# Optimization experiments

Hardware: AMD Instinct MI355X
Metric: run time of the kernel (lower is better)

Reference implementation:

```python
import jax, jax.numpy as jnp
import numpy as np

B, N, C = 2, 2048, 1024
H = 16
D = C // H
HID = 4 * C
EPS = 1e-5


def layernorm(x, g, b):
    mu = jnp.mean(x, axis=-1, keepdims=True)
    var = jnp.var(x, axis=-1, keepdims=True)
    return (x - mu) * jax.lax.rsqrt(var + EPS) * g + b


def setup_inputs() -> dict:
    key = jax.random.key(0)
    ks = jax.random.split(key, 8)
    s = lambda fan_in: 1.0 / np.sqrt(fan_in)
    return {
        "x": jax.random.normal(ks[0], (B, N, C), dtype=jnp.float32),
        "ln1_g": jnp.ones((C,), jnp.float32),
        "ln1_b": jnp.zeros((C,), jnp.float32),
        "w_qkv": jax.random.normal(ks[1], (C, 3 * C), jnp.float32) * s(C),
        "w_proj": jax.random.normal(ks[2], (C, C), jnp.float32) * s(C),
        "b_proj": jnp.zeros((C,), jnp.float32),
        "ln2_g": jnp.ones((C,), jnp.float32),
        "ln2_b": jnp.zeros((C,), jnp.float32),
        "w_fc1": jax.random.normal(ks[3], (C, HID), jnp.float32) * s(C),
        "b_fc1": jnp.zeros((HID,), jnp.float32),
        "w_fc2": jax.random.normal(ks[4], (HID, C), jnp.float32) * s(HID),
        "b_fc2": jnp.zeros((C,), jnp.float32),
        "metadata": 0,
        "thw_shape": 2048,
    }


def reference(x, ln1_g, ln1_b, w_qkv, w_proj, b_proj, ln2_g, ln2_b,
              w_fc1, b_fc1, w_fc2, b_fc2, metadata, thw_shape):
    scale = 1.0 / np.sqrt(D)
    # --- attention branch (pre-norm) ---
    xn = layernorm(x, ln1_g, ln1_b)
    qkv = (xn @ w_qkv).reshape(B, N, 3, H, D)
    q = jnp.transpose(qkv[:, :, 0], (0, 2, 1, 3))  # [B,H,N,D]
    k = jnp.transpose(qkv[:, :, 1], (0, 2, 1, 3))
    v = jnp.transpose(qkv[:, :, 2], (0, 2, 1, 3))
    attn = jax.nn.softmax(jnp.einsum('bhnd,bhmd->bhnm', q, k) * scale, axis=-1)
    o = jnp.einsum('bhnm,bhmd->bhnd', attn, v)
    o = jnp.transpose(o, (0, 2, 1, 3)).reshape(B, N, C)
    x = x + (o @ w_proj + b_proj)
    # --- MLP branch (pre-norm) ---
    xn2 = layernorm(x, ln2_g, ln2_b)
    h = jax.nn.gelu(xn2 @ w_fc1 + b_fc1, approximate=False)  # torch GELU = exact erf
    x = x + (h @ w_fc2 + b_fc2)
    return x
```

## Files before the change

kernel.cpp:

```cpp
#include <hip/hip_runtime.h>

#define B_   2
#define N_   2048
#define C_   1024
#define H_   16
#define D_   64
#define HID_ 4096
#define M_   (B_ * N_)

typedef __attribute__((ext_vector_type(8))) short bf16x8;
typedef __attribute__((ext_vector_type(4))) short short4v;
typedef __attribute__((ext_vector_type(4))) float f32x4;

__device__ __forceinline__ unsigned short f2bf(float f) {
  unsigned int u = __builtin_bit_cast(unsigned int, f);
  u += 0x7fffu + ((u >> 16) & 1u);
  return (unsigned short)(u >> 16);
}
__device__ __forceinline__ float bf2f(unsigned short s) {
  unsigned int u = ((unsigned int)s) << 16;
  return __builtin_bit_cast(float, u);
}
__device__ __forceinline__ unsigned int pkbf(float lo, float hi) {
  return __builtin_amdgcn_perm(__builtin_bit_cast(unsigned int, hi),
                               __builtin_bit_cast(unsigned int, lo),
                               0x07060302u);
}

__device__ __forceinline__ void gl2lds16(const void* g, void* l) {
  __builtin_amdgcn_global_load_lds(
      (const __attribute__((address_space(1))) unsigned int*)g,
      (__attribute__((address_space(3))) unsigned int*)l, 16, 0, 0);
}

__global__ __launch_bounds__(256) void ln_kernel(const float* __restrict__ x,
                                                 const float* __restrict__ g,
                                                 const float* __restrict__ bta,
                                                 unsigned short* __restrict__ out) {
  int row  = blockIdx.x * 4 + (threadIdx.x >> 6);
  int lane = threadIdx.x & 63;
  const float* xr = x + (size_t)row * C_;
  float4 v[4];
  float s1 = 0.f, s2 = 0.f;
#pragma unroll
  for (int j = 0; j < 4; j++) {
    v[j] = *(const float4*)(xr + j * 256 + lane * 4);
    s1 += v[j].x + v[j].y + v[j].z + v[j].w;
    s2 += v[j].x * v[j].x + v[j].y * v[j].y + v[j].z * v[j].z + v[j].w * v[j].w;
  }
#pragma unroll
  for (int m = 1; m < 64; m <<= 1) { s1 += __shfl_xor(s1, m); s2 += __shfl_xor(s2, m); }
  float mu  = s1 * (1.0f / C_);
  float var = s2 * (1.0f / C_) - mu * mu;
  float rs  = rsqrtf(var + 1e-5f);
#pragma unroll
  for (int j = 0; j < 4; j++) {
    const float4 gv = *(const float4*)(g + j * 256 + lane * 4);
    const float4 bv = *(const float4*)(bta + j * 256 + lane * 4);
    ushort4 o;
    o.x = f2bf((v[j].x - mu) * rs * gv.x + bv.x);
    o.y = f2bf((v[j].y - mu) * rs * gv.y + bv.y);
    o.z = f2bf((v[j].z - mu) * rs * gv.z + bv.z);
    o.w = f2bf((v[j].w - mu) * rs * gv.w + bv.w);
    *(ushort4*)(out + (size_t)row * C_ + j * 256 + lane * 4) = o;
  }
}

__global__ __launch_bounds__(256) void wtrans_kernel(const float* __restrict__ W,
                                                     unsigned short* __restrict__ Wt,
                                                     int K, int N) {
  __shared__ float t[32][33];
  int n0 = blockIdx.x * 32, k0 = blockIdx.y * 32;
  int tx = threadIdx.x, ty = threadIdx.y;
#pragma unroll
  for (int j = 0; j < 4; j++)
    t[ty + j * 8][tx] = W[(size_t)(k0 + ty + j * 8) * N + n0 + tx];
  __syncthreads();
#pragma unroll
  for (int j = 0; j < 4; j++)
    Wt[(size_t)(n0 + ty + j * 8) * K + k0 + tx] = f2bf(t[tx][ty + j * 8]);
}

__global__ __launch_bounds__(256) void vtrans_kernel(const unsigned short* __restrict__ v,
                                                     unsigned short* __restrict__ vt) {
  __shared__ unsigned short t[32][33];
  int bh = blockIdx.z;
  int n0 = blockIdx.x * 32, d0 = blockIdx.y * 32;
  const unsigned short* src = v + (size_t)bh * N_ * D_;
  unsigned short* dst = vt + (size_t)bh * D_ * N_;
  int tx = threadIdx.x, ty = threadIdx.y;
#pragma unroll
  for (int j = 0; j < 4; j++)
    t[ty + j * 8][tx] = src[(size_t)(n0 + ty + j * 8) * D_ + d0 + tx];
  __syncthreads();
#pragma unroll
  for (int j = 0; j < 4; j++)
    dst[(size_t)(d0 + ty + j * 8) * N_ + n0 + tx] = t[tx][ty + j * 8];
}

template <int MODE, int BN>
__global__ __launch_bounds__(256) void gemm_kernel(
    const unsigned short* __restrict__ A,
    const unsigned short* __restrict__ Wt,
    const float* __restrict__ bias,
    const float* __restrict__ resid,
    float* __restrict__ outf,
    float* __restrict__ partf,
    unsigned short* __restrict__ outb0,
    unsigned short* __restrict__ outb1,
    unsigned short* __restrict__ outb2,
    int M, int N, int K) {
  constexpr int MT = (BN == 128) ? 4 : 2;
  __shared__ __align__(16) short As[128][64];
  __shared__ __align__(16) short Bs[BN][64];
  int tid = threadIdx.x;
  int w = tid >> 6, lane = tid & 63, r = lane & 15, quad = lane >> 4;
  int rowbase = (BN == 128) ? (w >> 1) * 64 : w * 32;
  int colbase = (BN == 128) ? (w & 1) * 64 : 0;
  int bM = blockIdx.y * 128, bN = blockIdx.x * BN;

  int kz   = (MODE == 3) ? blockIdx.z : 0;
  int kbeg = (MODE == 3) ? kz * (K >> 1) : 0;
  int kend = (MODE == 3) ? kbeg + (K >> 1) : K;

  int srow   = (w << 3) + (lane >> 3);
  int schunk = (lane & 7) ^ ((lane >> 3) & 7);
  const unsigned short* aP = A  + (size_t)(bM + srow) * K + schunk * 8;
  const unsigned short* bP = Wt + (size_t)(bN + srow) * K + schunk * 8;

  int pc0 = (quad ^ (r & 7)) * 8;

  f32x4 acc[MT][4];
#pragma unroll
  for (int i = 0; i < MT; i++)
#pragma unroll
    for (int j = 0; j < 4; j++) acc[i][j] = f32x4{0.f, 0.f, 0.f, 0.f};

  for (int k0 = kbeg; k0 < kend; k0 += 64) {
    __syncthreads();
#pragma unroll
    for (int p = 0; p < 4; p++)
      gl2lds16(aP + (size_t)(p * 32) * K + k0, &As[p * 32 + (w << 3)][0]);
#pragma unroll
    for (int p = 0; p < BN / 32; p++)
      gl2lds16(bP + (size_t)(p * 32) * K + k0, &Bs[p * 32 + (w << 3)][0]);
    __syncthreads();
#pragma unroll
    for (int kh = 0; kh < 2; kh++) {
      int pc = pc0 ^ (kh * 32);
      bf16x8 af[MT], bfr[4];
#pragma unroll
      for (int mt = 0; mt < MT; mt++)
        af[mt] = *(const bf16x8*)&As[rowbase + mt * 16 + r][pc];
#pragma unroll
      for (int nt = 0; nt < 4; nt++)
        bfr[nt] = *(const bf16x8*)&Bs[colbase + nt * 16 + r][pc];
#pragma unroll
      for (int mt = 0; mt < MT; mt++)
#pragma unroll
        for (int nt = 0; nt < 4; nt++)
          acc[mt][nt] = __builtin_amdgcn_mfma_f32_16x16x32_bf16(af[mt], bfr[nt], acc[mt][nt], 0, 0, 0);
    }
  }

#pragma unroll
  for (int mt = 0; mt < MT; mt++) {
#pragma unroll
    for (int nt = 0; nt < 4; nt++) {
#pragma unroll
      for (int i = 0; i < 4; i++) {
        int gm = bM + rowbase + mt * 16 + quad * 4 + i;
        int gn = bN + colbase + nt * 16 + r;
        float val = acc[mt][nt][i];
        if (MODE == 0) {
          int s = gn >> 10, c = gn & 1023;
          int hh = c >> 6, d = c & 63;
          int b = gm >> 11, n = gm & 2047;
          size_t di = ((size_t)(b * H_ + hh) * N_ + n) * D_ + d;
          unsigned short bvv = f2bf(s == 0 ? val * 0.125f : val);
          (s == 0 ? outb0 : (s == 1 ? outb1 : outb2))[di] = bvv;
        } else if (MODE == 1) {
          outf[(size_t)gm * N + gn] = val + bias[gn] + resid[(size_t)gm * N + gn];
        } else if (MODE == 2) {
          float t = val + bias[gn];
          float gl = 0.5f * t * (1.0f + erff(t * 0.70710678118f));
          outb0[(size_t)gm * N + gn] = f2bf(gl);
        } else {
          if (kz == 0)
            outf[(size_t)gm * N + gn] = val + bias[gn] + resid[(size_t)gm * N + gn];
          else
            partf[(size_t)gm * N + gn] = val;
        }
      }
    }
  }
}

__global__ __launch_bounds__(256) void addpart_kernel(float* __restrict__ out,
                                                      const float* __restrict__ part) {
  int i = blockIdx.x * 256 + threadIdx.x;
  float4 a = *(const float4*)(out + (size_t)i * 4);
  float4 b = *(const float4*)(part + (size_t)i * 4);
  a.x += b.x; a.y += b.y; a.z += b.z; a.w += b.w;
  *(float4*)(out + (size_t)i * 4) = a;
}

__global__ __launch_bounds__(256) void attn_kernel(const unsigned short* __restrict__ qb,
                                                   const unsigned short* __restrict__ kb,
                                                   const unsigned short* __restrict__ vtb,
                                                   unsigned short* __restrict__ Op,
                                                   float2* __restrict__ ml) {
  __shared__ __align__(16) short Kbuf[2][128][64];
  __shared__ __align__(16) short Vbuf[2][64][128];
  __shared__ __align__(16) short Pl[4][16][128];
  int tid = threadIdx.x;
  int w = tid >> 6, lane = tid & 63, r = lane & 15, quad = lane >> 4;
  int kbi = blockIdx.x & 1;
  int idx = blockIdx.x >> 1;
  int bh = idx >> 4, qt = idx & 15;
  const unsigned short* qh  = qb  + (size_t)bh * N_ * D_;
  const unsigned short* kh  = kb  + (size_t)bh * N_ * D_;
  const unsigned short* vth = vtb + (size_t)bh * D_ * N_;

  bf16x8 qf[2][2];
#pragma unroll
  for (int mt = 0; mt < 2; mt++)
#pragma unroll
    for (int ks = 0; ks < 2; ks++)
      qf[mt][ks] = *(const bf16x8*)(qh + (size_t)(qt * 128 + w * 32 + mt * 16 + r) * D_ + ks * 32 + quad * 8);

  float lst[2] = {0.f, 0.f};
  f32x4 oacc[2][4];
#pragma unroll
  for (int mt = 0; mt < 2; mt++)
#pragma unroll
    for (int nt = 0; nt < 4; nt++) oacc[mt][nt] = f32x4{0.f, 0.f, 0.f, 0.f};

  int krow   = (w << 3) + (lane >> 3);
  int kchunk = (lane & 7) ^ ((lane >> 3) & 7);
  const unsigned short* kP = kh + (size_t)krow * D_ + kchunk * 8;
  int vrow   = (w << 2) + (lane >> 4);
  int vchunk = (lane & 15) ^ (vrow & 7);
  const unsigned short* vP = vth + (size_t)vrow * N_ + vchunk * 8;

  short* Plw = &Pl[w][0][0];
  int swz = (r & 7);
  int t0 = kbi * 8;

#pragma unroll
  for (int p = 0; p < 4; p++)
    gl2lds16(kP + (size_t)(t0 * 128 + p * 32) * D_, &Kbuf[0][p * 32 + (w << 3)][0]);
#pragma unroll
  for (int p = 0; p < 4; p++)
    gl2lds16(vP + (size_t)(p * 16) * N_ + t0 * 128, &Vbuf[0][p * 16 + (w << 2)][0]);

  for (int i = 0; i < 8; i++) {
    int bi = i & 1;
    __syncthreads();
    if (i + 1 < 8) {
      int tn = t0 + i + 1;
#pragma unroll
      for (int p = 0; p < 4; p++)
        gl2lds16(kP + (size_t)(tn * 128 + p * 32) * D_, &Kbuf[bi ^ 1][p * 32 + (w << 3)][0]);
#pragma unroll
      for (int p = 0; p < 4; p++)
        gl2lds16(vP + (size_t)(p * 16) * N_ + tn * 128, &Vbuf[bi ^ 1][p * 16 + (w << 2)][0]);
    }

    f32x4 sacc[2][8];
#pragma unroll
    for (int mt = 0; mt < 2; mt++)
#pragma unroll
      for (int nt = 0; nt < 8; nt++) sacc[mt][nt] = f32x4{0.f, 0.f, 0.f, 0.f};
#pragma unroll
    for (int ks = 0; ks < 2; ks++) {
#pragma unroll
      for (int nt = 0; nt < 8; nt++) {
        bf16x8 kfr = *(const bf16x8*)&Kbuf[bi][nt * 16 + r][((ks * 4 + quad) ^ swz) * 8];
#pragma unroll
        for (int mt = 0; mt < 2; mt++)
          sacc[mt][nt] = __builtin_amdgcn_mfma_f32_16x16x32_bf16(kfr, qf[mt][ks], sacc[mt][nt], 0, 0, 0);
      }
    }

#pragma unroll
    for (int mt = 0; mt < 2; mt++) {
      float rs = 0.f;
#pragma unroll
      for (int nt = 0; nt < 8; nt++)
#pragma unroll
        for (int i2 = 0; i2 < 4; i2++) {
          float p = __expf(sacc[mt][nt][i2]);
          sacc[mt][nt][i2] = p;
          rs += p;
        }
      rs += __shfl_xor(rs, 16);
      rs += __shfl_xor(rs, 32);
      lst[mt] += rs;
    }

#pragma unroll
    for (int mt = 0; mt < 2; mt++) {
#pragma unroll
      for (int nt = 0; nt < 8; nt++) {
        uint2 pk;
        pk.x = pkbf(sacc[mt][nt][0], sacc[mt][nt][1]);
        pk.y = pkbf(sacc[mt][nt][2], sacc[mt][nt][3]);
        *(uint2*)&Plw[r * 128 + (((nt * 2 + (quad >> 1)) ^ swz) * 8) + (quad & 1) * 4] = pk;
      }
      asm volatile("" ::: "memory");
#pragma unroll
      for (int ks = 0; ks < 4; ks++) {
        bf16x8 pfr = *(const bf16x8*)&Plw[r * 128 + ((ks * 4 + quad) ^ swz) * 8];
#pragma unroll
        for (int nt2 = 0; nt2 < 4; nt2++) {
          bf16x8 vfr = *(const bf16x8*)&Vbuf[bi][nt2 * 16 + r][((ks * 4 + quad) ^ swz) * 8];
          oacc[mt][nt2] = __builtin_amdgcn_mfma_f32_16x16x32_bf16(pfr, vfr, oacc[mt][nt2], 0, 0, 0);
        }
      }
      asm volatile("" ::: "memory");
    }
  }

  size_t base = ((size_t)(kbi * 32 + bh)) * N_;
#pragma unroll
  for (int mt = 0; mt < 2; mt++) {
    if (quad == 0) {
      int row = qt * 128 + w * 32 + mt * 16 + r;
      ml[base + row] = float2{0.f, lst[mt]};
    }
#pragma unroll
    for (int i = 0; i < 4; i++) {
      float li = __shfl(lst[mt], (lane & 48) | (quad * 4 + i));
      float inv = 1.0f / li;
      int row = qt * 128 + w * 32 + mt * 16 + quad * 4 + i;
#pragma unroll
      for (int nt2 = 0; nt2 < 4; nt2++) {
        int d = nt2 * 16 + r;
        Op[(base + row) * D_ + d] = f2bf(oacc[mt][nt2][i] * inv);
      }
    }
  }
}

__global__ __launch_bounds__(256) void attn_combine_kernel(const unsigned short* __restrict__ Op,
                                                           const float2* __restrict__ ml,
                                                           unsigned short* __restrict__ ob) {
  int gid = blockIdx.x * 256 + threadIdx.x;
  int row = gid >> 3;
  int dq  = (gid & 7) << 3;
  int bh = row >> 11, n = row & 2047;
  int bb = bh >> 4, hh = bh & 15;
  float2 a0 = ml[row];
  float2 a1 = ml[(size_t)B_ * H_ * N_ + row];
  float m = fmaxf(a0.x, a1.x);
  float w0 = __expf(a0.x - m) * a0.y;
  float w1 = __expf(a1.x - m) * a1.y;
  float inv = 1.0f / (w0 + w1);
  w0 *= inv; w1 *= inv;
  const ushort4 o0  = *(const ushort4*)(Op + (size_t)row * D_ + dq);
  const ushort4 o0b = *(const ushort4*)(Op + (size_t)row * D_ + dq + 4);
  const ushort4 o1  = *(const ushort4*)(Op + ((size_t)B_ * H_ * N_ + row) * D_ + dq);
  const ushort4 o1b = *(const ushort4*)(Op + ((size_t)B_ * H_ * N_ + row) * D_ + dq + 4);
  ushort4 r0, r1;
  r0.x = f2bf(w0 * bf2f(o0.x) + w1 * bf2f(o1.x));
  r0.y = f2bf(w0 * bf2f(o0.y) + w1 * bf2f(o1.y));
  r0.z = f2bf(w0 * bf2f(o0.z) + w1 * bf2f(o1.z));
  r0.w = f2bf(w0 * bf2f(o0.w) + w1 * bf2f(o1.w));
  r1.x = f2bf(w0 * bf2f(o0b.x) + w1 * bf2f(o1b.x));
  r1.y = f2bf(w0 * bf2f(o0b.y) + w1 * bf2f(o1b.y));
  r1.z = f2bf(w0 * bf2f(o0b.z) + w1 * bf2f(o1b.z));
  r1.w = f2bf(w0 * bf2f(o0b.w) + w1 * bf2f(o1b.w));
  unsigned short* dst = ob + ((size_t)bb * N_ + n) * C_ + hh * D_ + dq;
  *(ushort4*)dst = r0;
  *(ushort4*)(dst + 4) = r1;
}

extern "C" void kernel_launch(void* const* d_in, const int* in_sizes, int n_in,
                              void* d_out, int out_size, void* d_ws, size_t ws_size,
                              hipStream_t stream) {
  const float* x     = (const float*)d_in[0];
  const float* ln1g  = (const float*)d_in[1];
  const float* ln1b  = (const float*)d_in[2];
  const float* wqkv  = (const float*)d_in[3];
  const float* wproj = (const float*)d_in[4];
  const float* bproj = (const float*)d_in[5];
  const float* ln2g  = (const float*)d_in[6];
  const float* ln2b  = (const float*)d_in[7];
  const float* wfc1  = (const float*)d_in[8];
  const float* bfc1  = (const float*)d_in[9];
  const float* wfc2  = (const float*)d_in[10];
  const float* bfc2  = (const float*)d_in[11];
  float* out = (float*)d_out;

  const size_t MB = 1u << 20;
  if (ws_size < 88 * MB) return;
  char* w = (char*)d_ws;
  unsigned short* xn    = (unsigned short*)(w + 0 * MB);
  float2*         mlbuf = (float2*)        (w + 0 * MB);
  unsigned short* qbuf  = (unsigned short*)(w + 8 * MB);
  unsigned short* kbuf  = (unsigned short*)(w + 16 * MB);
  unsigned short* vbuf  = (unsigned short*)(w + 24 * MB);
  unsigned short* hbuf  = (unsigned short*)(w + 0 * MB);
  unsigned short* obuf  = (unsigned short*)(w + 32 * MB);
  float*          x2    = (float*)         (w + 40 * MB);
  unsigned short* opart = (unsigned short*)(w + 40 * MB);
  unsigned short* xn2   = (unsigned short*)(w + 56 * MB);
  unsigned short* vtb   = (unsigned short*)(w + 56 * MB);
  unsigned short* wqkvt = (unsigned short*)(w + 64 * MB);
  float*          partf = (float*)         (w + 64 * MB);
  unsigned short* wprjt = (unsigned short*)(w + 70 * MB);
  unsigned short* wfc1t = (unsigned short*)(w + 72 * MB);
  unsigned short* wfc2t = (unsigned short*)(w + 80 * MB);

  dim3 tb(32, 8);
  ln_kernel<<<M_ / 4, 256, 0, stream>>>(x, ln1g, ln1b, xn);
  wtrans_kernel<<<dim3(3 * C_ / 32, C_ / 32), tb, 0, stream>>>(wqkv, wqkvt, C_, 3 * C_);
  wtrans_kernel<<<dim3(C_ / 32, C_ / 32), tb, 0, stream>>>(wproj, wprjt, C_, C_);
  wtrans_kernel<<<dim3(HID_ / 32, C_ / 32), tb, 0, stream>>>(wfc1, wfc1t, C_, HID_);
  wtrans_kernel<<<dim3(C_ / 32, HID_ / 32), tb, 0, stream>>>(wfc2, wfc2t, HID_, C_);

  gemm_kernel<0, 128><<<dim3(3 * C_ / 128, M_ / 128), 256, 0, stream>>>(
      xn, wqkvt, nullptr, nullptr, nullptr, nullptr, qbuf, kbuf, vbuf, M_, 3 * C_, C_);
  vtrans_kernel<<<dim3(N_ / 32, D_ / 32, B_ * H_), tb, 0, stream>>>(vbuf, vtb);
  attn_kernel<<<B_ * H_ * (N_ / 128) * 2, 256, 0, stream>>>(qbuf, kbuf, vtb, opart, mlbuf);
  attn_combine_kernel<<<B_ * H_ * N_ * 8 / 256, 256, 0, stream>>>(opart, mlbuf, obuf);
  gemm_kernel<1, 64><<<dim3(C_ / 64, M_ / 128), 256, 0, stream>>>(
      obuf, wprjt, bproj, x, x2, nullptr, nullptr, nullptr, nullptr, M_, C_, C_);
  ln_kernel<<<M_ / 4, 256, 0, stream>>>(x2, ln2g, ln2b, xn2);
  gemm_kernel<2, 128><<<dim3(HID_ / 128, M_ / 128), 256, 0, stream>>>(
      xn2, wfc1t, bfc1, nullptr, nullptr, nullptr, hbuf, nullptr, nullptr, M_, HID_, C_);
  gemm_kernel<3, 128><<<dim3(C_ / 128, M_ / 128, 2), 256, 0, stream>>>(
      hbuf, wfc2t, bfc2, x2, out, partf, nullptr, nullptr, nullptr, M_, C_, HID_);
  addpart_kernel<<<M_ * C_ / 1024, 256, 0, stream>>>(out, partf);
}
```

Baseline: 399.6 us.

## Drop attention split-KV and combine kernel; merge weight transposes into one launch

Attention now has each block walk all 16 key tiles instead of splitting keys across two blocks. This removes the partial-output and max/sum buffers and the separate combine kernel, and the normalized result is written straight into the [B,N,C] layout. The trade is half as many attention blocks (512), which lowers parallelism and occupancy on the GPU. Separately, the four weight-transpose launches are merged into a single launch that picks the matrix by block index, saving launch overhead.

```diff
diff --git a/kernel.cpp b/kernel.cpp
--- a/kernel.cpp
+++ b/kernel.cpp
@@ -9,17 +9,12 @@
 #define M_   (B_ * N_)
 
 typedef __attribute__((ext_vector_type(8))) short bf16x8;
-typedef __attribute__((ext_vector_type(4))) short short4v;
 typedef __attribute__((ext_vector_type(4))) float f32x4;
 
 __device__ __forceinline__ unsigned short f2bf(float f) {
   unsigned int u = __builtin_bit_cast(unsigned int, f);
   u += 0x7fffu + ((u >> 16) & 1u);
   return (unsigned short)(u >> 16);
-}
-__device__ __forceinline__ float bf2f(unsigned short s) {
-  unsigned int u = ((unsigned int)s) << 16;
-  return __builtin_bit_cast(float, u);
 }
 __device__ __forceinline__ unsigned int pkbf(float lo, float hi) {
   return __builtin_amdgcn_perm(__builtin_bit_cast(unsigned int, hi),
@@ -66,11 +61,20 @@
   }
 }
 
-__global__ __launch_bounds__(256) void wtrans_kernel(const float* __restrict__ W,
-                                                     unsigned short* __restrict__ Wt,
-                                                     int K, int N) {
+__global__ __launch_bounds__(256) void wtrans_all_kernel(
+    const float* __restrict__ W0, unsigned short* __restrict__ T0,
+    const float* __restrict__ W1, unsigned short* __restrict__ T1,
+    const float* __restrict__ W2, unsigned short* __restrict__ T2,
+    const float* __restrict__ W3, unsigned short* __restrict__ T3) {
   __shared__ float t[32][33];
-  int n0 = blockIdx.x * 32, k0 = blockIdx.y * 32;
+  int id = blockIdx.x;
+  const float* W; unsigned short* T; int K, N, tile;
+  if (id < 3072)        { W = W0; T = T0; K = 1024; N = 3072; tile = id; }
+  else if (id < 4096)   { W = W1; T = T1; K = 1024; N = 1024; tile = id - 3072; }
+  else if (id < 8192)   { W = W2; T = T2; K = 1024; N = 4096; tile = id - 4096; }
+  else                  { W = W3; T = T3; K = 4096; N = 1024; tile = id - 8192; }
+  int nx = N >> 5;
+  int n0 = (tile % nx) * 32, k0 = (tile / nx) * 32;
   int tx = threadIdx.x, ty = threadIdx.y;
 #pragma unroll
   for (int j = 0; j < 4; j++)
@@ -78,7 +82,7 @@
   __syncthreads();
 #pragma unroll
   for (int j = 0; j < 4; j++)
-    Wt[(size_t)(n0 + ty + j * 8) * K + k0 + tx] = f2bf(t[tx][ty + j * 8]);
+    T[(size_t)(n0 + ty + j * 8) * K + k0 + tx] = f2bf(t[tx][ty + j * 8]);
 }
 
 __global__ __launch_bounds__(256) void vtrans_kernel(const unsigned short* __restrict__ v,
@@ -208,15 +212,13 @@
 __global__ __launch_bounds__(256) void attn_kernel(const unsigned short* __restrict__ qb,
                                                    const unsigned short* __restrict__ kb,
                                                    const unsigned short* __restrict__ vtb,
-                                                   unsigned short* __restrict__ Op,
-                                                   float2* __restrict__ ml) {
+                                                   unsigned short* __restrict__ ob) {
   __shared__ __align__(16) short Kbuf[2][128][64];
   __shared__ __align__(16) short Vbuf[2][64][128];
   __shared__ __align__(16) short Pl[4][16][128];
   int tid = threadIdx.x;
   int w = tid >> 6, lane = tid & 63, r = lane & 15, quad = lane >> 4;
-  int kbi = blockIdx.x & 1;
-  int idx = blockIdx.x >> 1;
+  int idx = blockIdx.x;
   int bh = idx >> 4, qt = idx & 15;
   const unsigned short* qh  = qb  + (size_t)bh * N_ * D_;
   const unsigned short* kh  = kb  + (size_t)bh * N_ * D_;
@@ -245,20 +247,19 @@
 
   short* Plw = &Pl[w][0][0];
   int swz = (r & 7);
-  int t0 = kbi * 8;
 
 #pragma unroll
   for (int p = 0; p < 4; p++)
-    gl2lds16(kP + (size_t)(t0 * 128 + p * 32) * D_, &Kbuf[0][p * 32 + (w << 3)][0]);
+    gl2lds16(kP + (size_t)(p * 32) * D_, &Kbuf[0][p * 32 + (w << 3)][0]);
 #pragma unroll
   for (int p = 0; p < 4; p++)
-    gl2lds16(vP + (size_t)(p * 16) * N_ + t0 * 128, &Vbuf[0][p * 16 + (w << 2)][0]);
-
-  for (int i = 0; i < 8; i++) {
-    int bi = i & 1;
+    gl2lds16(vP + (size_t)(p * 16) * N_, &Vbuf[0][p * 16 + (w << 2)][0]);
+
+  for (int t = 0; t < 16; t++) {
+    int bi = t & 1;
     __syncthreads();
-    if (i + 1 < 8) {
-      int tn = t0 + i + 1;
+    if (t + 1 < 16) {
+      int tn = t + 1;
 #pragma unroll
       for (int p = 0; p < 4; p++)
         gl2lds16(kP + (size_t)(tn * 128 + p * 32) * D_, &Kbuf[bi ^ 1][p * 32 + (w << 3)][0]);
@@ -322,13 +323,9 @@
     }
   }
 
-  size_t base = ((size_t)(kbi * 32 + bh)) * N_;
+  int bb = bh >> 4, hh = bh & 15;
 #pragma unroll
   for (int mt = 0; mt < 2; mt++) {
-    if (quad == 0) {
-      int row = qt * 128 + w * 32 + mt * 16 + r;
-      ml[base + row] = float2{0.f, lst[mt]};
-    }
 #pragma unroll
     for (int i = 0; i < 4; i++) {
       float li = __shfl(lst[mt], (lane & 48) | (quad * 4 + i));
@@ -337,43 +334,10 @@
 #pragma unroll
       for (int nt2 = 0; nt2 < 4; nt2++) {
         int d = nt2 * 16 + r;
-        Op[(base + row) * D_ + d] = f2bf(oacc[mt][nt2][i] * inv);
-      }
-    }
-  }
-}
-
-__global__ __launch_bounds__(256) void attn_combine_kernel(const unsigned short* __restrict__ Op,
-                                                           const float2* __restrict__ ml,
-                                                           unsigned short* __restrict__ ob) {
-  int gid = blockIdx.x * 256 + threadIdx.x;
-  int row = gid >> 3;
-  int dq  = (gid & 7) << 3;
-  int bh = row >> 11, n = row & 2047;
-  int bb = bh >> 4, hh = bh & 15;
-  float2 a0 = ml[row];
-  float2 a1 = ml[(size_t)B_ * H_ * N_ + row];
-  float m = fmaxf(a0.x, a1.x);
-  float w0 = __expf(a0.x - m) * a0.y;
-  float w1 = __expf(a1.x - m) * a1.y;
-  float inv = 1.0f / (w0 + w1);
-  w0 *= inv; w1 *= inv;
-  const ushort4 o0  = *(const ushort4*)(Op + (size_t)row * D_ + dq);
-  const ushort4 o0b = *(const ushort4*)(Op + (size_t)row * D_ + dq + 4);
-  const ushort4 o1  = *(const ushort4*)(Op + ((size_t)B_ * H_ * N_ + row) * D_ + dq);
-  const ushort4 o1b = *(const ushort4*)(Op + ((size_t)B_ * H_ * N_ + row) * D_ + dq + 4);
-  ushort4 r0, r1;
-  r0.x = f2bf(w0 * bf2f(o0.x) + w1 * bf2f(o1.x));
-  r0.y = f2bf(w0 * bf2f(o0.y) + w1 * bf2f(o1.y));
-  r0.z = f2bf(w0 * bf2f(o0.z) + w1 * bf2f(o1.z));
-  r0.w = f2bf(w0 * bf2f(o0.w) + w1 * bf2f(o1.w));
-  r1.x = f2bf(w0 * bf2f(o0b.x) + w1 * bf2f(o1b.x));
-  r1.y = f2bf(w0 * bf2f(o0b.y) + w1 * bf2f(o1b.y));
-  r1.z = f2bf(w0 * bf2f(o0b.z) + w1 * bf2f(o1b.z));
-  r1.w = f2bf(w0 * bf2f(o0b.w) + w1 * bf2f(o1b.w));
-  unsigned short* dst = ob + ((size_t)bb * N_ + n) * C_ + hh * D_ + dq;
-  *(ushort4*)dst = r0;
-  *(ushort4*)(dst + 4) = r1;
+        ob[((size_t)bb * N_ + row) * C_ + hh * D_ + d] = f2bf(oacc[mt][nt2][i] * inv);
+      }
+    }
+  }
 }
 
 extern "C" void kernel_launch(void* const* d_in, const int* in_sizes, int n_in,
@@ -397,14 +361,12 @@
   if (ws_size < 88 * MB) return;
   char* w = (char*)d_ws;
   unsigned short* xn    = (unsigned short*)(w + 0 * MB);
-  float2*         mlbuf = (float2*)        (w + 0 * MB);
   unsigned short* qbuf  = (unsigned short*)(w + 8 * MB);
   unsigned short* kbuf  = (unsigned short*)(w + 16 * MB);
   unsigned short* vbuf  = (unsigned short*)(w + 24 * MB);
   unsigned short* hbuf  = (unsigned short*)(w + 0 * MB);
   unsigned short* obuf  = (unsigned short*)(w + 32 * MB);
   float*          x2    = (float*)         (w + 40 * MB);
-  unsigned short* opart = (unsigned short*)(w + 40 * MB);
   unsigned short* xn2   = (unsigned short*)(w + 56 * MB);
   unsigned short* vtb   = (unsigned short*)(w + 56 * MB);
   unsigned short* wqkvt = (unsigned short*)(w + 64 * MB);
@@ -415,16 +377,13 @@
 
   dim3 tb(32, 8);
   ln_kernel<<<M_ / 4, 256, 0, stream>>>(x, ln1g, ln1b, xn);
-  wtrans_kernel<<<dim3(3 * C_ / 32, C_ / 32), tb, 0, stream>>>(wqkv, wqkvt, C_, 3 * C_);
-  wtrans_kernel<<<dim3(C_ / 32, C_ / 32), tb, 0, stream>>>(wproj, wprjt, C_, C_);
-  wtrans_kernel<<<dim3(HID_ / 32, C_ / 32), tb, 0, stream>>>(wfc1, wfc1t, C_, HID_);
-  wtrans_kernel<<<dim3(C_ / 32, HID_ / 32), tb, 0, stream>>>(wfc2, wfc2t, HID_, C_);
+  wtrans_all_kernel<<<12288, tb, 0, stream>>>(wqkv, wqkvt, wproj, wprjt,
+                                              wfc1, wfc1t, wfc2, wfc2t);
 
   gemm_kernel<0, 128><<<dim3(3 * C_ / 128, M_ / 128), 256, 0, stream>>>(
       xn, wqkvt, nullptr, nullptr, nullptr, nullptr, qbuf, kbuf, vbuf, M_, 3 * C_, C_);
   vtrans_kernel<<<dim3(N_ / 32, D_ / 32, B_ * H_), tb, 0, stream>>>(vbuf, vtb);
-  attn_kernel<<<B_ * H_ * (N_ / 128) * 2, 256, 0, stream>>>(qbuf, kbuf, vtb, opart, mlbuf);
-  attn_combine_kernel<<<B_ * H_ * N_ * 8 / 256, 256, 0, stream>>>(opart, mlbuf, obuf);
+  attn_kernel<<<B_ * H_ * (N_ / 128), 256, 0, stream>>>(qbuf, kbuf, vtb, obuf);
   gemm_kernel<1, 64><<<dim3(C_ / 64, M_ / 128), 256, 0, stream>>>(
       obuf, wprjt, bproj, x, x2, nullptr, nullptr, nullptr, nullptr, M_, C_, C_);
   ln_kernel<<<M_ / 4, 256, 0, stream>>>(x2, ln2g, ln2b, xn2);
```

After: 390.6 us. -2.3%, faster.
